# Kernel tuning notes

Measured on AMD Instinct MI355X. Metric: run time of the kernel, lower is better.

The kernel has to match this reference:

```python
import jax, jax.numpy as jnp
import numpy as np

IN_F = 4096
OUT_F = 4096
GROUP = 64  # quant group size along axis=0 of the reshaped weight


def setup_inputs() -> dict:
    key = jax.random.key(0)
    k1, k2, k3, k4, k5 = jax.random.split(key, 5)
    n_groups = IN_F * OUT_F // GROUP  # 262144
    x = jax.random.normal(k1, (8, 512, IN_F), dtype=jnp.float32)
    # packed 4-bit codes: two codes per byte, split along axis 0 (pack_4bit_u8)
    W_q = jax.random.randint(k2, (GROUP // 2, n_groups), 0, 256, dtype=jnp.int32)
    # scale here is meta['scale'] = 1/raw_scale (the dequant multiplier)
    scale = jax.random.uniform(k3, (1, n_groups), dtype=jnp.float32, minval=1e-3, maxval=1e-2)
    zero = jax.random.uniform(k4, (1, n_groups), dtype=jnp.float32, minval=0.0, maxval=15.0)
    bias = jax.random.normal(k5, (OUT_F,), dtype=jnp.float32) * 0.01
    return {"x": x, "W_q": W_q, "scale": scale, "zero": zero, "bias": bias}


def _dequantize(W_q, scale, zero):
    # unpack_4bit_u8: cat([(p >> 4) & 0xF, p & 0xF], axis=0) -> [GROUP, n_groups]
    hi = (W_q >> 4) & 0xF
    lo = W_q & 0xF
    W_q_p = jnp.concatenate([hi, lo], axis=0).astype(jnp.float32)
    # (W_q - zero) * scale, then reshape back to [out_features, in_features]
    return ((W_q_p - zero) * scale).reshape(OUT_F, IN_F)


def reference(x, W_q, scale, zero, bias):
    W_est = _dequantize(W_q, scale, zero)  # [OUT_F, IN_F]
    out = jnp.einsum('bsi,oi->bso', x, W_est)  # x @ W.T
    return out + bias
```

## Files before the change

kernel.cpp:

```cpp
#include <hip/hip_runtime.h>
#include <hip/hip_bf16.h>
#include <stdint.h>


#define IN_F  4096
#define OUT_F 4096
#define MROWS 4096

#define BM 256
#define BN 256
#define BK 64
#define NT (IN_F / BK)

typedef __attribute__((ext_vector_type(8))) __bf16 bf16x8;
typedef __attribute__((ext_vector_type(4))) float f32x4;

__device__ __forceinline__ ushort f2bf(float f) {
    uint32_t u = __float_as_uint(f);
    u += 0x7fffu + ((u >> 16) & 1u);
    return (ushort)(u >> 16);
}

#define CONV_BLK (MROWS * IN_F / 4 / 256)
#define DQ_BLK   (32 * 262144 / 4 / 256)

__global__ void prep(const float* __restrict__ x, ushort* __restrict__ xb,
                     const int* __restrict__ Wq, const float* __restrict__ scale,
                     const float* __restrict__ zero, ushort* __restrict__ West) {
    int blk = blockIdx.x;
    if (blk < CONV_BLK) {
        int i = (blk * 256 + threadIdx.x) * 4;
        float4 v = *(const float4*)(x + i);
        *(ushort4*)(xb + i) = make_ushort4(f2bf(v.x), f2bf(v.y), f2bf(v.z), f2bf(v.w));
    } else {
        int t = (blk - CONV_BLK) * 256 + threadIdx.x;
        int flat = t << 2;
        int p = flat >> 18;
        int c = flat & 262143;
        int j = c >> 12;
        int i = c & 4095;

        int4 q = *(const int4*)(Wq + flat);
        float4 sc = *(const float4*)(scale + c);
        float4 zr = *(const float4*)(zero + c);

        int   qv[4] = {q.x, q.y, q.z, q.w};
        float sv[4] = {sc.x, sc.y, sc.z, sc.w};
        float zv[4] = {zr.x, zr.y, zr.z, zr.w};

        ushort hi[4], lo[4];
#pragma unroll
        for (int e = 0; e < 4; ++e) {
            hi[e] = f2bf(((float)((qv[e] >> 4) & 0xF) - zv[e]) * sv[e]);
            lo[e] = f2bf(((float)(qv[e] & 0xF) - zv[e]) * sv[e]);
        }
        size_t o_hi = (size_t)(p * 64 + j) * IN_F + i;
        size_t o_lo = (size_t)((p + 32) * 64 + j) * IN_F + i;
        *(ushort4*)(West + o_hi) = make_ushort4(hi[0], hi[1], hi[2], hi[3]);
        *(ushort4*)(West + o_lo) = make_ushort4(lo[0], lo[1], lo[2], lo[3]);
    }
}

__device__ __forceinline__ void gload16(const ushort* g, const ushort* l) {
    __builtin_amdgcn_global_load_lds((const __attribute__((address_space(1))) void*)g,
                                     (__attribute__((address_space(3))) void*)l,
                                     16, 0, 0);
}


#define VMCNT6 asm volatile("s_waitcnt vmcnt(6)" ::: "memory");
#define VMCNT0 asm volatile("s_waitcnt vmcnt(0)" ::: "memory");
#define BAR    __builtin_amdgcn_s_barrier();

#define DS_A(bb, kk, mh)                                                   \
    _Pragma("unroll") for (int mf = 0; mf < 4; ++mf)                       \
        afr[mf] = ap[bb][(kk) * 1024 + (mh) * 256 + mf * 64];

#define DS_B(bb, kk)                                                       \
    _Pragma("unroll") for (int nf = 0; nf < 4; ++nf)                       \
        bfr[nf] = bp[bb][(kk) * 1024 + nf * 64];

#define STAGE_A(nb, kh, kcol) {                                            \
    gload16(A + plA0 + (kcol), &lds[(nb)*32768 + (kh)*8192 + wave*512]);   \
    gload16(A + plA1 + (kcol), &lds[(nb)*32768 + (kh)*8192 + 4096 + wave*512]); }

#define STAGE_B(nb, kh, kcol) {                                            \
    gload16(B + plB0 + (kcol), &lds[(nb)*32768 + 16384 + (kh)*8192 + wave*512]); \
    gload16(B + plB1 + (kcol), &lds[(nb)*32768 + 16384 + (kh)*8192 + 4096 + wave*512]); }

#define MFMA16(mh)                                                                 \
    __builtin_amdgcn_s_setprio(1);                                                 \
    _Pragma("unroll") for (int mf = 0; mf < 4; ++mf)                               \
    _Pragma("unroll") for (int nf = 0; nf < 4; ++nf)                               \
        acc[(mh) * 4 + mf][nf] = __builtin_amdgcn_mfma_f32_16x16x32_bf16(          \
            afr[mf], bfr[nf], acc[(mh) * 4 + mf][nf], 0, 0, 0);                    \
    __builtin_amdgcn_s_setprio(0);

__global__ __launch_bounds__(512, 2) void gemm_bt(const ushort* __restrict__ A,
                                                  const ushort* __restrict__ B,
                                                  const float* __restrict__ bias,
                                                  float* __restrict__ C) {
    __shared__ alignas(16) ushort lds[65536];

    const int tid  = threadIdx.x;
    const int wave = tid >> 6;
    const int lane = tid & 63;
    const int rl   = lane & 15;
    const int hh   = lane >> 4;
    const int hx   = hh ^ ((rl >> 1) & 3);

    int bid = blockIdx.x;
    int swz = (bid & 7) * 32 + (bid >> 3);
    const int m0 = (swz >> 4) * BM;
    const int n0 = (swz & 15) * BN;
    const int wr = wave >> 2;
    const int wc = wave & 3;

    f32x4 acc[8][4];
    f32x4 z4 = {0.f, 0.f, 0.f, 0.f};
#pragma unroll
    for (int i = 0; i < 8; ++i)
#pragma unroll
        for (int j = 0; j < 4; ++j) acc[i][j] = z4;

    uint plA0, plA1, plB0, plB1;
    {
        int s0 = wave * 64 + lane, r0 = s0 >> 2, h0 = (s0 & 3) ^ ((r0 >> 1) & 3);
        int s1 = 512 + wave * 64 + lane, r1 = s1 >> 2, h1 = (s1 & 3) ^ ((r1 >> 1) & 3);
        plA0 = (uint)((m0 + r0) * IN_F + h0 * 8);
        plA1 = (uint)((m0 + r1) * IN_F + h1 * 8);
        plB0 = (uint)((n0 + r0) * IN_F + h0 * 8);
        plB1 = (uint)((n0 + r1) * IN_F + h1 * 8);
    }

    const uint abase = (uint)(((wr * 128 + rl) * 4 + hx) * 8);
    const uint bbase = (uint)(16384 + ((wc * 64 + rl) * 4 + hx) * 8);
    const bf16x8* ap[2] = { (const bf16x8*)&lds[abase],
                            (const bf16x8*)&lds[32768 + abase] };
    const bf16x8* bp[2] = { (const bf16x8*)&lds[bbase],
                            (const bf16x8*)&lds[32768 + bbase] };

    STAGE_A(0, 0, 0u)
    STAGE_B(0, 0, 0u)
    STAGE_A(0, 1, 32u)
    STAGE_B(0, 1, 32u)
    STAGE_A(1, 0, (uint)BK)
    VMCNT6;
    BAR;

#pragma unroll 1
    for (int T = 0; T < NT; T += 2) {
        const uint kn1 = (uint)(((T + 1) & (NT - 1)) * BK);
        const uint kn2 = (uint)(((T + 2) & (NT - 1)) * BK);
        const uint kn3 = (uint)(((T + 3) & (NT - 1)) * BK);
        bf16x8 afr[4], bfr[4];

        DS_B(0, 0) DS_A(0, 0, 0)
        STAGE_B(1, 0, kn1)
        BAR; MFMA16(0) BAR;

        DS_A(0, 0, 1)
        STAGE_A(1, 1, kn1 + 32)
        VMCNT6;
        BAR; MFMA16(1) BAR;

        DS_B(0, 1) DS_A(0, 1, 0)
        STAGE_B(1, 1, kn1 + 32)
        BAR; MFMA16(0) BAR;

        DS_A(0, 1, 1)
        STAGE_A(0, 0, kn2)
        VMCNT6;
        BAR; MFMA16(1) BAR;

        DS_B(1, 0) DS_A(1, 0, 0)
        STAGE_B(0, 0, kn2)
        BAR; MFMA16(0) BAR;

        DS_A(1, 0, 1)
        STAGE_A(0, 1, kn2 + 32)
        VMCNT6;
        BAR; MFMA16(1) BAR;

        DS_B(1, 1) DS_A(1, 1, 0)
        STAGE_B(0, 1, kn2 + 32)
        BAR; MFMA16(0) BAR;

        DS_A(1, 1, 1)
        STAGE_A(1, 0, kn3)
        VMCNT6;
        BAR; MFMA16(1) BAR;
    }
    VMCNT0;

#pragma unroll
    for (int nf = 0; nf < 4; ++nf) {
        int col = n0 + wc * 64 + nf * 16 + rl;
        float bv = bias[col];
#pragma unroll
        for (int mfa = 0; mfa < 8; ++mfa) {
            int rbase = m0 + wr * 128 + mfa * 16 + (hh << 2);
#pragma unroll
            for (int v = 0; v < 4; ++v)
                C[(size_t)(rbase + v) * OUT_F + col] = acc[mfa][nf][v] + bv;
        }
    }
}

extern "C" void kernel_launch(void* const* d_in, const int* in_sizes, int n_in,
                              void* d_out, int out_size, void* d_ws, size_t ws_size,
                              hipStream_t stream) {
    const float* x     = (const float*)d_in[0];
    const int*   Wq    = (const int*)d_in[1];
    const float* scale = (const float*)d_in[2];
    const float* zero  = (const float*)d_in[3];
    const float* bias  = (const float*)d_in[4];
    float* out = (float*)d_out;

    ushort* xb   = (ushort*)d_ws;
    ushort* West = (ushort*)d_ws + (size_t)MROWS * IN_F;

    prep<<<CONV_BLK + DQ_BLK, 256, 0, stream>>>(x, xb, Wq, scale, zero, West);
    gemm_bt<<<(MROWS / BM) * (OUT_F / BN), 512, 0, stream>>>(xb, West, bias, out);
}
```

Measured before the change: 270.6 us.

## Double-buffer MFMA register fragments to overlap LDS reads with compute

Fragments are now read from LDS one phase ahead into alternating register sets (af0/af1, bf0/bf1), so the ds_reads for the next MFMA block are issued before the current MFMA block. Sched barriers keep the compiler from reordering them across phases. The four global-load base offsets are folded into two plus a constant stride, which frees a few VGPRs. The extra fragment registers raise register pressure, which could cause spills or hurt the 2-blocks-per-CU occupancy, and the prefetch reads rely on the existing barrier and vmcnt placement to stay race-free.

```diff
diff --git a/kernel.cpp b/kernel.cpp
--- a/kernel.cpp
+++ b/kernel.cpp
@@ -71,29 +71,30 @@
 #define VMCNT6 asm volatile("s_waitcnt vmcnt(6)" ::: "memory");
 #define VMCNT0 asm volatile("s_waitcnt vmcnt(0)" ::: "memory");
 #define BAR    __builtin_amdgcn_s_barrier();
-
-#define DS_A(bb, kk, mh)                                                   \
+#define SB0    __builtin_amdgcn_sched_barrier(0);
+
+#define RD_A(bb, kk, mh, DST)                                              \
     _Pragma("unroll") for (int mf = 0; mf < 4; ++mf)                       \
-        afr[mf] = ap[bb][(kk) * 1024 + (mh) * 256 + mf * 64];
-
-#define DS_B(bb, kk)                                                       \
+        DST[mf] = ap[bb][(kk) * 1024 + (mh) * 256 + mf * 64];
+
+#define RD_B(bb, kk, DST)                                                  \
     _Pragma("unroll") for (int nf = 0; nf < 4; ++nf)                       \
-        bfr[nf] = bp[bb][(kk) * 1024 + nf * 64];
+        DST[nf] = bp[bb][(kk) * 1024 + nf * 64];
 
 #define STAGE_A(nb, kh, kcol) {                                            \
-    gload16(A + plA0 + (kcol), &lds[(nb)*32768 + (kh)*8192 + wave*512]);   \
-    gload16(A + plA1 + (kcol), &lds[(nb)*32768 + (kh)*8192 + 4096 + wave*512]); }
+    gload16(A + plA + (kcol), &lds[(nb)*32768 + (kh)*8192 + wave*512]);    \
+    gload16(A + plA + 524288u + (kcol), &lds[(nb)*32768 + (kh)*8192 + 4096 + wave*512]); }
 
 #define STAGE_B(nb, kh, kcol) {                                            \
-    gload16(B + plB0 + (kcol), &lds[(nb)*32768 + 16384 + (kh)*8192 + wave*512]); \
-    gload16(B + plB1 + (kcol), &lds[(nb)*32768 + 16384 + (kh)*8192 + 4096 + wave*512]); }
-
-#define MFMA16(mh)                                                                 \
+    gload16(B + plB + (kcol), &lds[(nb)*32768 + 16384 + (kh)*8192 + wave*512]); \
+    gload16(B + plB + 524288u + (kcol), &lds[(nb)*32768 + 16384 + (kh)*8192 + 4096 + wave*512]); }
+
+#define MFMA16(mh, AF, BF)                                                         \
     __builtin_amdgcn_s_setprio(1);                                                 \
     _Pragma("unroll") for (int mf = 0; mf < 4; ++mf)                               \
     _Pragma("unroll") for (int nf = 0; nf < 4; ++nf)                               \
         acc[(mh) * 4 + mf][nf] = __builtin_amdgcn_mfma_f32_16x16x32_bf16(          \
-            afr[mf], bfr[nf], acc[(mh) * 4 + mf][nf], 0, 0, 0);                    \
+            AF[mf], BF[nf], acc[(mh) * 4 + mf][nf], 0, 0, 0);                      \
     __builtin_amdgcn_s_setprio(0);
 
 __global__ __launch_bounds__(512, 2) void gemm_bt(const ushort* __restrict__ A,
@@ -123,14 +124,11 @@
 #pragma unroll
         for (int j = 0; j < 4; ++j) acc[i][j] = z4;
 
-    uint plA0, plA1, plB0, plB1;
+    uint plA, plB;
     {
         int s0 = wave * 64 + lane, r0 = s0 >> 2, h0 = (s0 & 3) ^ ((r0 >> 1) & 3);
-        int s1 = 512 + wave * 64 + lane, r1 = s1 >> 2, h1 = (s1 & 3) ^ ((r1 >> 1) & 3);
-        plA0 = (uint)((m0 + r0) * IN_F + h0 * 8);
-        plA1 = (uint)((m0 + r1) * IN_F + h1 * 8);
-        plB0 = (uint)((n0 + r0) * IN_F + h0 * 8);
-        plB1 = (uint)((n0 + r1) * IN_F + h1 * 8);
+        plA = (uint)((m0 + r0) * IN_F + h0 * 8);
+        plB = (uint)((n0 + r0) * IN_F + h0 * 8);
     }
 
     const uint abase = (uint)(((wr * 128 + rl) * 4 + hx) * 8);
@@ -139,6 +137,8 @@
                             (const bf16x8*)&lds[32768 + abase] };
     const bf16x8* bp[2] = { (const bf16x8*)&lds[bbase],
                             (const bf16x8*)&lds[32768 + bbase] };
+
+    bf16x8 af0[4], af1[4], bf0[4], bf1[4];
 
     STAGE_A(0, 0, 0u)
     STAGE_B(0, 0, 0u)
@@ -147,49 +147,50 @@
     STAGE_A(1, 0, (uint)BK)
     VMCNT6;
     BAR;
+    RD_B(0, 0, bf0)
+    RD_A(0, 0, 0, af0)
 
 #pragma unroll 1
     for (int T = 0; T < NT; T += 2) {
         const uint kn1 = (uint)(((T + 1) & (NT - 1)) * BK);
         const uint kn2 = (uint)(((T + 2) & (NT - 1)) * BK);
         const uint kn3 = (uint)(((T + 3) & (NT - 1)) * BK);
-        bf16x8 afr[4], bfr[4];
-
-        DS_B(0, 0) DS_A(0, 0, 0)
+
+        RD_A(0, 0, 1, af1)
         STAGE_B(1, 0, kn1)
-        BAR; MFMA16(0) BAR;
-
-        DS_A(0, 0, 1)
+        SB0 BAR; MFMA16(0, af0, bf0) BAR;
+
         STAGE_A(1, 1, kn1 + 32)
         VMCNT6;
-        BAR; MFMA16(1) BAR;
-
-        DS_B(0, 1) DS_A(0, 1, 0)
+        RD_B(0, 1, bf1) RD_A(0, 1, 0, af0)
+        SB0 BAR; MFMA16(1, af1, bf0) BAR;
+
+        RD_A(0, 1, 1, af1)
         STAGE_B(1, 1, kn1 + 32)
-        BAR; MFMA16(0) BAR;
-
-        DS_A(0, 1, 1)
+        SB0 BAR; MFMA16(0, af0, bf1) BAR;
+
         STAGE_A(0, 0, kn2)
         VMCNT6;
-        BAR; MFMA16(1) BAR;
-
-        DS_B(1, 0) DS_A(1, 0, 0)
+        RD_B(1, 0, bf0) RD_A(1, 0, 0, af0)
+        SB0 BAR; MFMA16(1, af1, bf1) BAR;
+
+        RD_A(1, 0, 1, af1)
         STAGE_B(0, 0, kn2)
-        BAR; MFMA16(0) BAR;
-
-        DS_A(1, 0, 1)
+        SB0 BAR; MFMA16(0, af0, bf0) BAR;
+
         STAGE_A(0, 1, kn2 + 32)
         VMCNT6;
-        BAR; MFMA16(1) BAR;
-
-        DS_B(1, 1) DS_A(1, 1, 0)
+        RD_B(1, 1, bf1) RD_A(1, 1, 0, af0)
+        SB0 BAR; MFMA16(1, af1, bf0) BAR;
+
+        RD_A(1, 1, 1, af1)
         STAGE_B(0, 1, kn2 + 32)
-        BAR; MFMA16(0) BAR;
-
-        DS_A(1, 1, 1)
+        SB0 BAR; MFMA16(0, af0, bf1) BAR;
+
         STAGE_A(1, 0, kn3)
         VMCNT6;
-        BAR; MFMA16(1) BAR;
+        RD_B(0, 0, bf0) RD_A(0, 0, 0, af0)
+        SB0 BAR; MFMA16(1, af1, bf1) BAR;
     }
     VMCNT0;
 
```

After: 269.4 us. About the same (-0.5%).
